# Performance work log

Measured on AMD Instinct MI355X. Metric: run time of the kernel, lower is better.

The kernel has to match this reference:

```python
import jax, jax.numpy as jnp
import numpy as np

B, N, T, DIN = 64, 512, 8, 2
H, L, E, M, P = 256, 3, 8192, 128, 12
EPS = 1e-5


def setup_inputs() -> dict:
    key = jax.random.key(0)
    ks = jax.random.split(key, 10)
    obs_traj = jax.random.normal(ks[0], (B, N, T, DIN), dtype=jnp.float32)
    nodes = jax.random.randint(ks[1], (B, 1, E), 0, N)
    edges = jax.random.randint(ks[2], (B, 1, E), 0, M)
    hyperedge_indices = jnp.concatenate([nodes, edges], axis=1)  # [B,2,E]
    s = 0.05
    return {
        "obs_traj": obs_traj,
        "hyperedge_indices": hyperedge_indices,
        "W_enc": jax.random.normal(ks[3], (DIN, H), dtype=jnp.float32) * s,
        "b_enc": jnp.zeros((H,), dtype=jnp.float32),
        "thetas": jax.random.normal(ks[4], (L, H, H), dtype=jnp.float32) * s,
        "conv_biases": jnp.zeros((L, H), dtype=jnp.float32),
        "gammas": jnp.ones((L, H), dtype=jnp.float32),
        "betas": jnp.zeros((L, H), dtype=jnp.float32),
        "W_dec": jax.random.normal(ks[5], (H, P * 2), dtype=jnp.float32) * s,
        "b_dec": jnp.zeros((P * 2,), dtype=jnp.float32),
    }


def _hconv(x, idx, theta, bias):
    # PyG HypergraphConv: out = D^{-1} H B^{-1} H^T (X Theta) + bias
    # x: [N,H], idx: [2,E] (row0 node ids, row1 hyperedge ids)
    nodes, edges = idx[0], idx[1]
    xt = x @ theta  # [N,H]
    ones = jnp.ones((idx.shape[1],), dtype=x.dtype)
    b_deg = jax.ops.segment_sum(ones, edges, num_segments=M)  # hyperedge degree [M]
    d_deg = jax.ops.segment_sum(ones, nodes, num_segments=N)  # node degree [N]
    msg = jax.ops.segment_sum(xt[nodes], edges, num_segments=M)  # [M,H]
    msg = msg / jnp.maximum(b_deg, 1.0)[:, None]
    out = jax.ops.segment_sum(msg[edges], nodes, num_segments=N)  # [N,H]
    out = out / jnp.maximum(d_deg, 1.0)[:, None]
    return out + bias


def reference(obs_traj, hyperedge_indices, W_enc, b_enc, thetas, conv_biases,
              gammas, betas, W_dec, b_dec):
    # TemporalEncoder: per-step linear + ReLU, mean over time -> [B,N,H]
    h = jnp.mean(jax.nn.relu(obs_traj @ W_enc + b_enc), axis=2)
    h_social = h
    for l in range(L):
        conv = jax.vmap(lambda x, idx: _hconv(x, idx, thetas[l], conv_biases[l]))
        hc = conv(h_social, hyperedge_indices)  # [B,N,H]
        # BatchNorm1d applied per sample (training-mode stats over node dim)
        mu = jnp.mean(hc, axis=1, keepdims=True)
        var = jnp.var(hc, axis=1, keepdims=True)
        hn = (hc - mu) * jax.lax.rsqrt(var + EPS) * gammas[l] + betas[l]
        h_social = jax.nn.relu(hn)  # dropout = identity (eval)
    h_combined = h + h_social
    out = h_combined @ W_dec + b_dec  # [B,N,P*2]
    return out.reshape(B, N, P, 2)
```

## Files before the change

kernel.cpp:

```cpp
#include <hip/hip_runtime.h>
#include <hip/hip_bf16.h>

#define B_   64
#define N_   512
#define T_   8
#define DIN_ 2
#define H_   256
#define L_   3
#define E_   8192
#define M_   128
#define P2_  24
#define EPS_ 1e-5f

#define WTPAD 136

typedef __attribute__((ext_vector_type(8))) short short8;
typedef __attribute__((ext_vector_type(4))) float floatx4;

__device__ __forceinline__ unsigned short f2bf(float f) {
    union { float f; unsigned u; } v; v.f = f;
    unsigned r = v.u + 0x7FFF + ((v.u >> 16) & 1);
    return (unsigned short)(r >> 16);
}
__device__ __forceinline__ float bf2f(unsigned short h) {
    union { unsigned u; float f; } v; v.u = (unsigned)h << 16; return v.f;
}

__global__ __launch_bounds__(512, 4) void prep_kernel(
    const float* __restrict__ obs, const float* __restrict__ Wenc,
    const float* __restrict__ benc,
    unsigned short* __restrict__ actT, long actLo,
    const int* __restrict__ idx, unsigned short* __restrict__ Hmat,
    unsigned short* __restrict__ HmatT, float* __restrict__ DinvN,
    float* __restrict__ degM,
    const float* __restrict__ thetas, unsigned short* __restrict__ thT, long thLo)
{
    __shared__ __align__(16) char u[33024];
    int bid = blockIdx.x, tid = threadIdx.x;
    if (bid < 256) {
        float* ot = (float*)u;
        int x8 = bid & 7, s = bid >> 3;
        int b = ((s >> 2) << 3) | x8;
        int h0 = (s & 3) * 64;
        const float4* src = (const float4*)(obs + (long)b * N_ * 16);
        for (int i = tid; i < 2048; i += 512) {
            float4 v = src[i];
            int n = i >> 2, k4 = (i & 3) << 2;
            ot[(k4 + 0) * 513 + n] = v.x;
            ot[(k4 + 1) * 513 + n] = v.y;
            ot[(k4 + 2) * 513 + n] = v.z;
            ot[(k4 + 3) * 513 + n] = v.w;
        }
        __syncthreads();
        int wave = tid >> 6, lane = tid & 63;
        int cbase = h0 + wave * 8;
        float w0[8], w1[8], bb[8];
#pragma unroll
        for (int i = 0; i < 8; ++i) {
            w0[i] = Wenc[cbase + i];
            w1[i] = Wenc[H_ + cbase + i];
            bb[i] = benc[cbase + i];
        }
        for (int j = 0; j < 8; ++j) {
            int n = j * 64 + lane;
            float x0[8], x1[8];
#pragma unroll
            for (int t = 0; t < 8; ++t) {
                x0[t] = ot[(2 * t) * 513 + n];
                x1[t] = ot[(2 * t + 1) * 513 + n];
            }
#pragma unroll
            for (int i = 0; i < 8; ++i) {
                float acc = 0.f;
#pragma unroll
                for (int t = 0; t < 8; ++t)
                    acc += fmaxf(x0[t] * w0[i] + x1[t] * w1[i] + bb[i], 0.f);
                acc *= 0.125f;
                long o = ((long)b * H_ + cbase + i) * N_ + n;
                unsigned short hv = f2bf(acc);
                actT[o] = hv;
                actT[actLo + o] = f2bf(acc - bf2f(hv));
            }
        }
    } else if (bid < 768) {
        unsigned* cnt = (unsigned*)u;
        int id2 = bid - 256;
        int x8 = id2 & 7, s = id2 >> 3;
        int b = ((s >> 3) << 3) | x8;
        int chunk = s & 7;
        int c0 = chunk * 64;
        for (int i = tid; i < 64 * 129; i += 512) cnt[i] = 0;
        __syncthreads();
        const int* nodes = idx + (long)b * 2 * E_;
        const int* edges = nodes + E_;
        for (int e = tid; e < E_; e += 512) {
            int n = nodes[e];
            if ((n >> 6) == chunk) atomicAdd(&cnt[(n & 63) * 129 + edges[e]], 1u);
        }
        __syncthreads();
        for (int i = tid; i < 64 * 128; i += 512) {
            int r = i >> 7, m = i & 127;
            Hmat[((long)(b * N_ + c0 + r)) * M_ + m] = f2bf((float)cnt[r * 129 + m]);
        }
        for (int i = tid; i < 64 * 128; i += 512) {
            int m = i >> 6, r = i & 63;
            HmatT[((long)(b * M_ + m)) * N_ + c0 + r] = f2bf((float)cnt[r * 129 + m]);
        }
        if (tid < 64) {
            unsigned s2 = 0;
#pragma unroll 8
            for (int m = 0; m < 128; ++m) s2 += cnt[tid * 129 + m];
            DinvN[b * N_ + c0 + tid] = 1.0f / fmaxf((float)s2, 1.0f);
        } else if (tid < 192) {
            int m = tid - 64;
            unsigned s2 = 0;
#pragma unroll 8
            for (int r = 0; r < 64; ++r) s2 += cnt[r * 129 + m];
            atomicAdd(&degM[b * M_ + m], (float)s2);
        }
    } else {
        float (*tile)[65] = (float(*)[65])u;
        int sub = bid - 768;
        int cx = sub & 3, ry = (sub >> 2) & 3, l = sub >> 4;
        int r0 = ry * 64, c0 = cx * 64;
        const float* ib = thetas + (long)l * H_ * H_;
        unsigned short* ob = thT + (long)l * H_ * H_;
        int x = tid & 63, y0 = tid >> 6;
#pragma unroll
        for (int i = 0; i < 8; ++i) {
            int y = y0 * 8 + i;
            tile[y][x] = ib[(long)(r0 + y) * H_ + c0 + x];
        }
        __syncthreads();
#pragma unroll
        for (int i = 0; i < 8; ++i) {
            int y = y0 * 8 + i;
            float v = tile[x][y];
            unsigned short hv = f2bf(v);
            long o = (long)(c0 + y) * H_ + r0 + x;
            ob[o] = hv;
            ob[thLo + o] = f2bf(v - bf2f(hv));
        }
    }
}

__global__ __launch_bounds__(256, 4) void z_kernel(
    const unsigned short* __restrict__ HmatT,
    const unsigned short* __restrict__ actIn, long actLo,
    const float* __restrict__ degM,
    unsigned short* __restrict__ Zg, long zLo)
{
    __shared__ __align__(16) unsigned short As1[128 * 40];
    __shared__ __align__(16) unsigned short Bh[64 * 40];
    __shared__ __align__(16) unsigned short Bl[64 * 40];
    int b = blockIdx.x, hs = blockIdx.y * 64;
    int tid = threadIdx.x, wave = tid >> 6, lane = tid & 63;
    int lr = lane & 15, lq = lane >> 4;
    int wm = (wave & 1) * 64, wn = (wave >> 1) * 32;
    const unsigned short* HT   = HmatT + (long)b * M_ * N_;
    const unsigned short* aInH = actIn + (long)b * H_ * N_ + (long)hs * N_;
    const unsigned short* aInL = actIn + actLo + (long)b * H_ * N_ + (long)hs * N_;

    floatx4 acc[4][2] = {};
    int r0 = tid >> 2, ck = (tid & 3) << 3;
    int r1 = r0 + 64;
    uint4 pA0 = *(const uint4*)&HT[(long)r0 * N_ + ck];
    uint4 pA1 = *(const uint4*)&HT[(long)r1 * N_ + ck];
    uint4 pBh = *(const uint4*)&aInH[(long)r0 * N_ + ck];
    uint4 pBl = *(const uint4*)&aInL[(long)r0 * N_ + ck];
    for (int k0 = 0; k0 < N_; k0 += 32) {
        __syncthreads();
        *(uint4*)&As1[r0 * 40 + ck] = pA0;
        *(uint4*)&As1[r1 * 40 + ck] = pA1;
        *(uint4*)&Bh[r0 * 40 + ck]  = pBh;
        *(uint4*)&Bl[r0 * 40 + ck]  = pBl;
        __syncthreads();
        int kn = k0 + 32;
        if (kn < N_) {
            pA0 = *(const uint4*)&HT[(long)r0 * N_ + kn + ck];
            pA1 = *(const uint4*)&HT[(long)r1 * N_ + kn + ck];
            pBh = *(const uint4*)&aInH[(long)r0 * N_ + kn + ck];
            pBl = *(const uint4*)&aInL[(long)r0 * N_ + kn + ck];
        }
        short8 af[4], bh[2], bl[2];
#pragma unroll
        for (int mt = 0; mt < 4; ++mt)
            af[mt] = *(const short8*)&As1[(wm + mt * 16 + lr) * 40 + lq * 8];
#pragma unroll
        for (int nt = 0; nt < 2; ++nt) {
            bh[nt] = *(const short8*)&Bh[(wn + nt * 16 + lr) * 40 + lq * 8];
            bl[nt] = *(const short8*)&Bl[(wn + nt * 16 + lr) * 40 + lq * 8];
        }
#pragma unroll
        for (int mt = 0; mt < 4; ++mt)
#pragma unroll
            for (int nt = 0; nt < 2; ++nt) {
                acc[mt][nt] = __builtin_amdgcn_mfma_f32_16x16x32_bf16(
                    af[mt], bh[nt], acc[mt][nt], 0, 0, 0);
                acc[mt][nt] = __builtin_amdgcn_mfma_f32_16x16x32_bf16(
                    af[mt], bl[nt], acc[mt][nt], 0, 0, 0);
            }
    }
#pragma unroll
    for (int mt = 0; mt < 4; ++mt)
#pragma unroll
        for (int r4 = 0; r4 < 4; ++r4) {
            int m = wm + mt * 16 + lq * 4 + r4;
            float rsB = 1.0f / fmaxf(degM[b * M_ + m], 1.0f);
#pragma unroll
            for (int nt = 0; nt < 2; ++nt) {
                float v = acc[mt][nt][r4] * rsB;
                unsigned short hv = f2bf(v);
                long o = ((long)b * M_ + m) * H_ + hs + wn + nt * 16 + lr;
                Zg[o] = hv;
                Zg[zLo + o] = f2bf(v - bf2f(hv));
            }
        }
}

__global__ __launch_bounds__(512, 4) void wh_kernel(
    const unsigned short* __restrict__ Zg, long zLo,
    const unsigned short* __restrict__ Hmat,
    const unsigned short* __restrict__ thT, long thLo,
    const float* __restrict__ DinvN, const float* __restrict__ convb,
    const float* __restrict__ gamma, const float* __restrict__ beta,
    unsigned short* __restrict__ actOut, long actLo)
{
    __shared__ __align__(16) char lds[28160];
    unsigned short* Zch  = (unsigned short*)lds;
    unsigned short* Zcl  = Zch + 128 * 40;
    unsigned short* As2h = Zcl + 128 * 40;
    unsigned short* As2l = As2h + 32 * 40;
    unsigned short* Wh   = (unsigned short*)lds;
    unsigned short* Wl   = Wh + 32 * WTPAD;
    float* rsum = (float*)(lds + 25600);
    float* rsq  = rsum + 256;
    float2* prm = (float2*)(rsq + 256);

    int id = blockIdx.x;
    int xcd = id & 7, slot = id >> 3;
    int chunk = slot & 7;
    int b  = ((slot >> 3) << 3) | xcd;
    int h0 = chunk * 32;

    int tid = threadIdx.x, wave = tid >> 6, lane = tid & 63;
    int lr = lane & 15, lq = lane >> 4;
    const unsigned short* Zb = Zg + (long)b * M_ * H_;
    const unsigned short* Hm = Hmat + (long)b * N_ * M_;

    int wm2 = (wave >> 2) * 16, wn2 = (wave & 3) * 32;
    int i2 = tid & 255, pl2 = tid >> 8;
    int r2 = i2 >> 2, ck2 = (i2 & 3) << 3;
    bool thAct = (i2 < 128);
    const unsigned short* thBase = thT + (pl2 ? thLo : 0) + (long)(h0 + r2) * H_ + ck2;
    unsigned short* As2dst = (pl2 ? As2l : As2h) + r2 * 40 + ck2;
    int rz = tid >> 2, ckz = (tid & 3) << 3;
    uint4 pTh = {};
    if (thAct) pTh = *(const uint4*)thBase;
    uint4 pZh = *(const uint4*)&Zb[(long)rz * H_ + ckz];
    uint4 pZl = *(const uint4*)&Zb[zLo + (long)rz * H_ + ckz];
    floatx4 acc2[2] = {};
    for (int k0 = 0; k0 < H_; k0 += 32) {
        __syncthreads();
        if (thAct) *(uint4*)As2dst = pTh;
        *(uint4*)&Zch[rz * 40 + ckz] = pZh;
        *(uint4*)&Zcl[rz * 40 + ckz] = pZl;
        __syncthreads();
        int kn = k0 + 32;
        if (kn < H_) {
            if (thAct) pTh = *(const uint4*)(thBase + kn);
            pZh = *(const uint4*)&Zb[(long)rz * H_ + kn + ckz];
            pZl = *(const uint4*)&Zb[zLo + (long)rz * H_ + kn + ckz];
        }
        short8 ah, al, zb[2], zl[2];
        ah = *(const short8*)&As2h[(wm2 + lr) * 40 + lq * 8];
        al = *(const short8*)&As2l[(wm2 + lr) * 40 + lq * 8];
#pragma unroll
        for (int nt = 0; nt < 2; ++nt) {
            zb[nt] = *(const short8*)&Zch[(wn2 + nt * 16 + lr) * 40 + lq * 8];
            zl[nt] = *(const short8*)&Zcl[(wn2 + nt * 16 + lr) * 40 + lq * 8];
        }
#pragma unroll
        for (int nt = 0; nt < 2; ++nt) {
            acc2[nt] = __builtin_amdgcn_mfma_f32_16x16x32_bf16(ah, zb[nt], acc2[nt], 0, 0, 0);
            acc2[nt] = __builtin_amdgcn_mfma_f32_16x16x32_bf16(ah, zl[nt], acc2[nt], 0, 0, 0);
            acc2[nt] = __builtin_amdgcn_mfma_f32_16x16x32_bf16(al, zb[nt], acc2[nt], 0, 0, 0);
        }
    }
    __syncthreads();
#pragma unroll
    for (int r4 = 0; r4 < 4; ++r4) {
        int row = wm2 + lq * 4 + r4;
#pragma unroll
        for (int nt = 0; nt < 2; ++nt) {
            int col = wn2 + nt * 16 + lr;
            float v = acc2[nt][r4];
            unsigned short hv = f2bf(v);
            Wh[row * WTPAD + col] = hv;
            Wl[row * WTPAD + col] = f2bf(v - bf2f(hv));
        }
    }
    __syncthreads();

    int wn3 = wave * 64;
    floatx4 acc3[2][4] = {};
    for (int k0 = 0; k0 < M_; k0 += 32) {
        short8 ah[2], al[2], bh3[4];
#pragma unroll
        for (int nt = 0; nt < 4; ++nt)
            bh3[nt] = *(const short8*)&Hm[(long)(wn3 + nt * 16 + lr) * M_ + k0 + lq * 8];
#pragma unroll
        for (int mt = 0; mt < 2; ++mt) {
            ah[mt] = *(const short8*)&Wh[(mt * 16 + lr) * WTPAD + k0 + lq * 8];
            al[mt] = *(const short8*)&Wl[(mt * 16 + lr) * WTPAD + k0 + lq * 8];
        }
#pragma unroll
        for (int mt = 0; mt < 2; ++mt)
#pragma unroll
            for (int nt = 0; nt < 4; ++nt) {
                acc3[mt][nt] = __builtin_amdgcn_mfma_f32_16x16x32_bf16(
                    ah[mt], bh3[nt], acc3[mt][nt], 0, 0, 0);
                acc3[mt][nt] = __builtin_amdgcn_mfma_f32_16x16x32_bf16(
                    al[mt], bh3[nt], acc3[mt][nt], 0, 0, 0);
            }
    }

    float dv[4];
#pragma unroll
    for (int nt = 0; nt < 4; ++nt)
        dv[nt] = DinvN[b * N_ + wn3 + nt * 16 + lr];
    float cb[2][4];
#pragma unroll
    for (int mt = 0; mt < 2; ++mt)
#pragma unroll
        for (int r4 = 0; r4 < 4; ++r4)
            cb[mt][r4] = convb[h0 + mt * 16 + lq * 4 + r4];
#pragma unroll
    for (int mt = 0; mt < 2; ++mt)
#pragma unroll
        for (int nt = 0; nt < 4; ++nt)
#pragma unroll
            for (int r4 = 0; r4 < 4; ++r4)
                acc3[mt][nt][r4] = acc3[mt][nt][r4] * dv[nt] + cb[mt][r4];

    float ps[2][4], pq[2][4];
#pragma unroll
    for (int mt = 0; mt < 2; ++mt)
#pragma unroll
        for (int r4 = 0; r4 < 4; ++r4) {
            float s = 0.f, q = 0.f;
#pragma unroll
            for (int nt = 0; nt < 4; ++nt) {
                float v = acc3[mt][nt][r4];
                s += v; q += v * v;
            }
            ps[mt][r4] = s; pq[mt][r4] = q;
        }
#pragma unroll
    for (int mask = 1; mask <= 8; mask <<= 1) {
#pragma unroll
        for (int mt = 0; mt < 2; ++mt)
#pragma unroll
            for (int r4 = 0; r4 < 4; ++r4) {
                ps[mt][r4] += __shfl_xor(ps[mt][r4], mask);
                pq[mt][r4] += __shfl_xor(pq[mt][r4], mask);
            }
    }
    if (lr == 0) {
#pragma unroll
        for (int mt = 0; mt < 2; ++mt)
#pragma unroll
            for (int r4 = 0; r4 < 4; ++r4) {
                int row = mt * 16 + lq * 4 + r4;
                rsum[row * 8 + wave] = ps[mt][r4];
                rsq[row * 8 + wave]  = pq[mt][r4];
            }
    }
    __syncthreads();
    if (tid < 32) {
        float s = 0.f, s2 = 0.f;
#pragma unroll
        for (int w = 0; w < 8; ++w) { s += rsum[tid * 8 + w]; s2 += rsq[tid * 8 + w]; }
        float mu  = s * (1.0f / N_);
        float var = fmaxf(s2 * (1.0f / N_) - mu * mu, 0.f);
        float sc  = gamma[h0 + tid] * rsqrtf(var + EPS_);
        prm[tid] = make_float2(sc, beta[h0 + tid] - mu * sc);
    }
    __syncthreads();

    unsigned short* ab = actOut + (long)b * H_ * N_;
#pragma unroll
    for (int mt = 0; mt < 2; ++mt)
#pragma unroll
        for (int r4 = 0; r4 < 4; ++r4) {
            int row = mt * 16 + lq * 4 + r4;
            float2 p = prm[row];
#pragma unroll
            for (int nt = 0; nt < 4; ++nt) {
                float y = fmaxf(acc3[mt][nt][r4] * p.x + p.y, 0.f);
                unsigned short hv = f2bf(y);
                long o = (long)(h0 + row) * N_ + wn3 + nt * 16 + lr;
                ab[o] = hv;
                ab[actLo + o] = f2bf(y - bf2f(hv));
            }
        }
}

__global__ __launch_bounds__(256, 2) void decoder_kernel(
    const unsigned short* __restrict__ hAct,
    const unsigned short* __restrict__ sAct,
    const float* __restrict__ Wdec, const float* __restrict__ bdec,
    float* __restrict__ out)
{
    __shared__ float ct[64 * 65];
    __shared__ float wd[256 * 25];
    int n0 = blockIdx.x * 64, b = blockIdx.y;
    int tid = threadIdx.x;
    for (int i = tid; i < 256 * 24; i += 256)
        wd[(i / 24) * 25 + (i % 24)] = Wdec[i];

    const unsigned short* hb = hAct + (long)b * H_ * N_;
    const unsigned short* sb = sAct + (long)b * H_ * N_;
    int x = tid & 63, y0 = tid >> 6;

    int n = tid >> 2;
    int p0 = (tid & 3) * 6;
    float acc[6] = {};

    for (int k0 = 0; k0 < H_; k0 += 64) {
        __syncthreads();
#pragma unroll
        for (int i = 0; i < 16; ++i) {
            int y = y0 * 16 + i;
            long o = (long)(k0 + y) * N_ + n0 + x;
            ct[x * 65 + y] = bf2f(hb[o]) + bf2f(sb[o]);
        }
        __syncthreads();
        const float* crow = &ct[n * 65];
#pragma unroll 8
        for (int kk = 0; kk < 64; ++kk) {
            float a = crow[kk];
            const float* wrow = &wd[(k0 + kk) * 25 + p0];
#pragma unroll
            for (int j = 0; j < 6; ++j)
                acc[j] += a * wrow[j];
        }
    }
    long ob = ((long)b * N_ + n0 + n) * P2_ + p0;
#pragma unroll
    for (int j = 0; j < 6; ++j)
        out[ob + j] = acc[j] + bdec[p0 + j];
}

extern "C" void kernel_launch(void* const* d_in, const int* in_sizes, int n_in,
                              void* d_out, int out_size, void* d_ws, size_t ws_size,
                              hipStream_t stream) {
    const float* obs    = (const float*)d_in[0];
    const int*   hyper  = (const int*)d_in[1];
    const float* Wenc   = (const float*)d_in[2];
    const float* benc   = (const float*)d_in[3];
    const float* thetas = (const float*)d_in[4];
    const float* convb  = (const float*)d_in[5];
    const float* gammas = (const float*)d_in[6];
    const float* betas  = (const float*)d_in[7];
    const float* Wdec   = (const float*)d_in[8];
    const float* bdec   = (const float*)d_in[9];
    float* out = (float*)d_out;

    char* w = (char*)d_ws;
    auto alloc = [&](size_t bytes) { char* p = w; w += (bytes + 255) & ~255ULL; return p; };
    float* DinvN = (float*)alloc((size_t)B_ * N_ * 4);
    float* degM  = (float*)alloc((size_t)B_ * M_ * 4);
    unsigned short* Hmat  = (unsigned short*)alloc((size_t)B_ * N_ * M_ * 2);
    unsigned short* HmatT = (unsigned short*)alloc((size_t)B_ * M_ * N_ * 2);
    unsigned short* act0  = (unsigned short*)alloc((size_t)B_ * H_ * N_ * 2 * 2);
    unsigned short* act1  = (unsigned short*)alloc((size_t)B_ * H_ * N_ * 2 * 2);
    unsigned short* act2  = (unsigned short*)alloc((size_t)B_ * H_ * N_ * 2 * 2);
    unsigned short* thT   = (unsigned short*)alloc((size_t)L_ * H_ * H_ * 2 * 2);
    unsigned short* Zg    = (unsigned short*)alloc((size_t)B_ * M_ * H_ * 2 * 2);

    const long actLo = (long)B_ * H_ * N_;
    const long thLo  = (long)L_ * H_ * H_;
    const long zLo   = (long)B_ * M_ * H_;

    hipMemsetAsync(degM, 0, (size_t)B_ * M_ * 4, stream);
    prep_kernel<<<816, 512, 0, stream>>>(
        obs, Wenc, benc, act0, actLo,
        hyper, Hmat, HmatT, DinvN, degM,
        thetas, thT, thLo);

    unsigned short* bufs[4] = { act0, act1, act2, act1 };
    for (int l = 0; l < L_; ++l) {
        z_kernel<<<dim3(B_, 4), 256, 0, stream>>>(
            HmatT, bufs[l], actLo, degM, Zg, zLo);
        wh_kernel<<<512, 512, 0, stream>>>(
            Zg, zLo, Hmat, thT + (size_t)l * H_ * H_, thLo,
            DinvN, convb + (size_t)l * H_,
            gammas + (size_t)l * H_, betas + (size_t)l * H_, bufs[l + 1], actLo);
    }
    decoder_kernel<<<dim3(8, B_), 256, 0, stream>>>(
        act0, bufs[L_], Wdec, bdec, out);
}
```

Baseline: 225.5 us.

## Fuse all stages into one persistent kernel with software grid barriers

```diff
diff --git a/kernel.cpp b/kernel.cpp
--- a/kernel.cpp
+++ b/kernel.cpp
@@ -13,6 +13,7 @@
 #define EPS_ 1e-5f
 
 #define WTPAD 136
+#define NBLK 512
 
 typedef __attribute__((ext_vector_type(8))) short short8;
 typedef __attribute__((ext_vector_type(4))) float floatx4;
@@ -26,430 +27,435 @@
     union { unsigned u; float f; } v; v.u = (unsigned)h << 16; return v.f;
 }
 
-__global__ __launch_bounds__(512, 4) void prep_kernel(
+__global__ __launch_bounds__(512, 4) void mega_kernel(
     const float* __restrict__ obs, const float* __restrict__ Wenc,
-    const float* __restrict__ benc,
-    unsigned short* __restrict__ actT, long actLo,
-    const int* __restrict__ idx, unsigned short* __restrict__ Hmat,
-    unsigned short* __restrict__ HmatT, float* __restrict__ DinvN,
-    float* __restrict__ degM,
-    const float* __restrict__ thetas, unsigned short* __restrict__ thT, long thLo)
+    const float* __restrict__ benc, const int* __restrict__ idx,
+    const float* __restrict__ thetas, const float* __restrict__ convb,
+    const float* __restrict__ gammas, const float* __restrict__ betas,
+    const float* __restrict__ Wdec, const float* __restrict__ bdec,
+    unsigned short* __restrict__ Hmat, unsigned short* __restrict__ HmatT,
+    float* __restrict__ DinvN, float* __restrict__ degM,
+    unsigned short* __restrict__ act0, unsigned short* __restrict__ act1,
+    unsigned short* __restrict__ act2, long actLo,
+    unsigned short* __restrict__ thT, long thLo,
+    unsigned short* __restrict__ Zg, long zLo,
+    unsigned* __restrict__ cnt, float* __restrict__ out)
 {
-    __shared__ __align__(16) char u[33024];
+    __shared__ __align__(16) char u[43008];
     int bid = blockIdx.x, tid = threadIdx.x;
-    if (bid < 256) {
-        float* ot = (float*)u;
-        int x8 = bid & 7, s = bid >> 3;
-        int b = ((s >> 2) << 3) | x8;
-        int h0 = (s & 3) * 64;
-        const float4* src = (const float4*)(obs + (long)b * N_ * 16);
-        for (int i = tid; i < 2048; i += 512) {
-            float4 v = src[i];
-            int n = i >> 2, k4 = (i & 3) << 2;
-            ot[(k4 + 0) * 513 + n] = v.x;
-            ot[(k4 + 1) * 513 + n] = v.y;
-            ot[(k4 + 2) * 513 + n] = v.z;
-            ot[(k4 + 3) * 513 + n] = v.w;
+    int wave = tid >> 6, lane = tid & 63;
+    int lr = lane & 15, lq = lane >> 4;
+    unsigned target = 0;
+
+    auto gbar = [&]() {
+        __syncthreads();
+        target += NBLK;
+        if (tid == 0) {
+            __threadfence();
+            atomicAdd(cnt, 1u);
+            while (atomicAdd(cnt, 0u) < target) __builtin_amdgcn_s_sleep(2);
+            __threadfence();
         }
         __syncthreads();
-        int wave = tid >> 6, lane = tid & 63;
-        int cbase = h0 + wave * 8;
-        float w0[8], w1[8], bb[8];
-#pragma unroll
-        for (int i = 0; i < 8; ++i) {
-            w0[i] = Wenc[cbase + i];
-            w1[i] = Wenc[H_ + cbase + i];
-            bb[i] = benc[cbase + i];
-        }
-        for (int j = 0; j < 8; ++j) {
-            int n = j * 64 + lane;
-            float x0[8], x1[8];
-#pragma unroll
-            for (int t = 0; t < 8; ++t) {
-                x0[t] = ot[(2 * t) * 513 + n];
-                x1[t] = ot[(2 * t + 1) * 513 + n];
-            }
+    };
+
+    for (int pass = 0; pass < 2; ++pass) {
+        int role = (pass == 0) ? bid : (bid < 304 ? 512 + bid : -1);
+        if (role < 0) break;
+        __syncthreads();
+        if (role < 256) {
+            float* ot = (float*)u;
+            int x8 = role & 7, s = role >> 3;
+            int b = ((s >> 2) << 3) | x8;
+            int h0 = (s & 3) * 64;
+            const float4* src = (const float4*)(obs + (long)b * N_ * 16);
+            for (int i = tid; i < 2048; i += 512) {
+                float4 v = src[i];
+                int n = i >> 2, k4 = (i & 3) << 2;
+                ot[(k4 + 0) * 513 + n] = v.x;
+                ot[(k4 + 1) * 513 + n] = v.y;
+                ot[(k4 + 2) * 513 + n] = v.z;
+                ot[(k4 + 3) * 513 + n] = v.w;
+            }
+            __syncthreads();
+            int cbase = h0 + wave * 8;
+            float w0[8], w1[8], bb[8];
 #pragma unroll
             for (int i = 0; i < 8; ++i) {
-                float acc = 0.f;
-#pragma unroll
-                for (int t = 0; t < 8; ++t)
-                    acc += fmaxf(x0[t] * w0[i] + x1[t] * w1[i] + bb[i], 0.f);
-                acc *= 0.125f;
-                long o = ((long)b * H_ + cbase + i) * N_ + n;
-                unsigned short hv = f2bf(acc);
-                actT[o] = hv;
-                actT[actLo + o] = f2bf(acc - bf2f(hv));
-            }
-        }
-    } else if (bid < 768) {
-        unsigned* cnt = (unsigned*)u;
-        int id2 = bid - 256;
-        int x8 = id2 & 7, s = id2 >> 3;
-        int b = ((s >> 3) << 3) | x8;
-        int chunk = s & 7;
-        int c0 = chunk * 64;
-        for (int i = tid; i < 64 * 129; i += 512) cnt[i] = 0;
-        __syncthreads();
-        const int* nodes = idx + (long)b * 2 * E_;
-        const int* edges = nodes + E_;
-        for (int e = tid; e < E_; e += 512) {
-            int n = nodes[e];
-            if ((n >> 6) == chunk) atomicAdd(&cnt[(n & 63) * 129 + edges[e]], 1u);
-        }
-        __syncthreads();
-        for (int i = tid; i < 64 * 128; i += 512) {
-            int r = i >> 7, m = i & 127;
-            Hmat[((long)(b * N_ + c0 + r)) * M_ + m] = f2bf((float)cnt[r * 129 + m]);
-        }
-        for (int i = tid; i < 64 * 128; i += 512) {
-            int m = i >> 6, r = i & 63;
-            HmatT[((long)(b * M_ + m)) * N_ + c0 + r] = f2bf((float)cnt[r * 129 + m]);
-        }
-        if (tid < 64) {
-            unsigned s2 = 0;
+                w0[i] = Wenc[cbase + i];
+                w1[i] = Wenc[H_ + cbase + i];
+                bb[i] = benc[cbase + i];
+            }
+            for (int j = 0; j < 8; ++j) {
+                int n = j * 64 + lane;
+                float x0[8], x1[8];
+#pragma unroll
+                for (int t = 0; t < 8; ++t) {
+                    x0[t] = ot[(2 * t) * 513 + n];
+                    x1[t] = ot[(2 * t + 1) * 513 + n];
+                }
+#pragma unroll
+                for (int i = 0; i < 8; ++i) {
+                    float acc = 0.f;
+#pragma unroll
+                    for (int t = 0; t < 8; ++t)
+                        acc += fmaxf(x0[t] * w0[i] + x1[t] * w1[i] + bb[i], 0.f);
+                    acc *= 0.125f;
+                    long o = ((long)b * H_ + cbase + i) * N_ + n;
+                    unsigned short hv = f2bf(acc);
+                    act0[o] = hv;
+                    act0[actLo + o] = f2bf(acc - bf2f(hv));
+                }
+            }
+        } else if (role < 768) {
+            unsigned* cw = (unsigned*)u;
+            int id2 = role - 256;
+            int x8 = id2 & 7, s = id2 >> 3;
+            int b = ((s >> 3) << 3) | x8;
+            int chunk = s & 7;
+            int c0 = chunk * 64;
+            for (int i = tid; i < 64 * 129; i += 512) cw[i] = 0;
+            __syncthreads();
+            const int* nodes = idx + (long)b * 2 * E_;
+            const int* edges = nodes + E_;
+            for (int e = tid; e < E_; e += 512) {
+                int n = nodes[e];
+                if ((n >> 6) == chunk) atomicAdd(&cw[(n & 63) * 129 + edges[e]], 1u);
+            }
+            __syncthreads();
+            for (int i = tid; i < 64 * 128; i += 512) {
+                int r = i >> 7, m = i & 127;
+                Hmat[((long)(b * N_ + c0 + r)) * M_ + m] = f2bf((float)cw[r * 129 + m]);
+            }
+            for (int i = tid; i < 64 * 128; i += 512) {
+                int m = i >> 6, r = i & 63;
+                HmatT[((long)(b * M_ + m)) * N_ + c0 + r] = f2bf((float)cw[r * 129 + m]);
+            }
+            if (tid < 64) {
+                unsigned s2 = 0;
 #pragma unroll 8
-            for (int m = 0; m < 128; ++m) s2 += cnt[tid * 129 + m];
-            DinvN[b * N_ + c0 + tid] = 1.0f / fmaxf((float)s2, 1.0f);
-        } else if (tid < 192) {
-            int m = tid - 64;
-            unsigned s2 = 0;
+                for (int m = 0; m < 128; ++m) s2 += cw[tid * 129 + m];
+                DinvN[b * N_ + c0 + tid] = 1.0f / fmaxf((float)s2, 1.0f);
+            } else if (tid < 192) {
+                int m = tid - 64;
+                unsigned s2 = 0;
 #pragma unroll 8
-            for (int r = 0; r < 64; ++r) s2 += cnt[r * 129 + m];
-            atomicAdd(&degM[b * M_ + m], (float)s2);
-        }
-    } else {
-        float (*tile)[65] = (float(*)[65])u;
-        int sub = bid - 768;
-        int cx = sub & 3, ry = (sub >> 2) & 3, l = sub >> 4;
-        int r0 = ry * 64, c0 = cx * 64;
-        const float* ib = thetas + (long)l * H_ * H_;
-        unsigned short* ob = thT + (long)l * H_ * H_;
-        int x = tid & 63, y0 = tid >> 6;
-#pragma unroll
-        for (int i = 0; i < 8; ++i) {
-            int y = y0 * 8 + i;
-            tile[y][x] = ib[(long)(r0 + y) * H_ + c0 + x];
-        }
-        __syncthreads();
-#pragma unroll
-        for (int i = 0; i < 8; ++i) {
-            int y = y0 * 8 + i;
-            float v = tile[x][y];
-            unsigned short hv = f2bf(v);
-            long o = (long)(c0 + y) * H_ + r0 + x;
-            ob[o] = hv;
-            ob[thLo + o] = f2bf(v - bf2f(hv));
+                for (int r = 0; r < 64; ++r) s2 += cw[r * 129 + m];
+                atomicAdd(&degM[b * M_ + m], (float)s2);
+            }
+        } else {
+            float (*tile)[65] = (float(*)[65])u;
+            int sub = role - 768;
+            int cx = sub & 3, ry = (sub >> 2) & 3, l = sub >> 4;
+            int r0 = ry * 64, c0 = cx * 64;
+            const float* ib = thetas + (long)l * H_ * H_;
+            unsigned short* ob = thT + (long)l * H_ * H_;
+            int x = tid & 63, y0 = tid >> 6;
+#pragma unroll
+            for (int i = 0; i < 8; ++i) {
+                int y = y0 * 8 + i;
+                tile[y][x] = ib[(long)(r0 + y) * H_ + c0 + x];
+            }
+            __syncthreads();
+#pragma unroll
+            for (int i = 0; i < 8; ++i) {
+                int y = y0 * 8 + i;
+                float v = tile[x][y];
+                unsigned short hv = f2bf(v);
+                long o = (long)(c0 + y) * H_ + r0 + x;
+                ob[o] = hv;
+                ob[thLo + o] = f2bf(v - bf2f(hv));
+            }
         }
     }
-}
-
-__global__ __launch_bounds__(256, 4) void z_kernel(
-    const unsigned short* __restrict__ HmatT,
-    const unsigned short* __restrict__ actIn, long actLo,
-    const float* __restrict__ degM,
-    unsigned short* __restrict__ Zg, long zLo)
-{
-    __shared__ __align__(16) unsigned short As1[128 * 40];
-    __shared__ __align__(16) unsigned short Bh[64 * 40];
-    __shared__ __align__(16) unsigned short Bl[64 * 40];
-    int b = blockIdx.x, hs = blockIdx.y * 64;
-    int tid = threadIdx.x, wave = tid >> 6, lane = tid & 63;
-    int lr = lane & 15, lq = lane >> 4;
-    int wm = (wave & 1) * 64, wn = (wave >> 1) * 32;
-    const unsigned short* HT   = HmatT + (long)b * M_ * N_;
-    const unsigned short* aInH = actIn + (long)b * H_ * N_ + (long)hs * N_;
-    const unsigned short* aInL = actIn + actLo + (long)b * H_ * N_ + (long)hs * N_;
-
-    floatx4 acc[4][2] = {};
-    int r0 = tid >> 2, ck = (tid & 3) << 3;
-    int r1 = r0 + 64;
-    uint4 pA0 = *(const uint4*)&HT[(long)r0 * N_ + ck];
-    uint4 pA1 = *(const uint4*)&HT[(long)r1 * N_ + ck];
-    uint4 pBh = *(const uint4*)&aInH[(long)r0 * N_ + ck];
-    uint4 pBl = *(const uint4*)&aInL[(long)r0 * N_ + ck];
-    for (int k0 = 0; k0 < N_; k0 += 32) {
-        __syncthreads();
-        *(uint4*)&As1[r0 * 40 + ck] = pA0;
-        *(uint4*)&As1[r1 * 40 + ck] = pA1;
-        *(uint4*)&Bh[r0 * 40 + ck]  = pBh;
-        *(uint4*)&Bl[r0 * 40 + ck]  = pBl;
-        __syncthreads();
-        int kn = k0 + 32;
-        if (kn < N_) {
-            pA0 = *(const uint4*)&HT[(long)r0 * N_ + kn + ck];
-            pA1 = *(const uint4*)&HT[(long)r1 * N_ + kn + ck];
-            pBh = *(const uint4*)&aInH[(long)r0 * N_ + kn + ck];
-            pBl = *(const uint4*)&aInL[(long)r0 * N_ + kn + ck];
+    gbar();
+
+    unsigned short* bufs[4] = { act0, act1, act2, act1 };
+    for (int l = 0; l < L_; ++l) {
+        {
+            unsigned short* As1 = (unsigned short*)u;
+            unsigned short* Bh  = As1 + 128 * 40;
+            unsigned short* Bl  = Bh + 32 * 40;
+            int x8 = bid & 7, slot = bid >> 3;
+            int b = ((slot >> 3) << 3) | x8;
+            int hs = (slot & 7) * 32;
+            const unsigned short* HT = HmatT + (long)b * M_ * N_;
+            const unsigned short* aH = bufs[l] + (long)b * H_ * N_ + (long)hs * N_;
+            const unsigned short* aL = bufs[l] + actLo + (long)b * H_ * N_ + (long)hs * N_;
+            int wm = (wave & 3) * 32, wn16 = (wave >> 2) * 16;
+            floatx4 acc[2] = {};
+            bool isA = tid < 256;
+            int r0 = (tid & 255) >> 2, c0 = (tid & 3) << 3;
+            int jb = tid - 256, plb = (jb >> 7) & 1, jj = jb & 127;
+            int rb = jj >> 2, cbb = (jj & 3) << 3;
+            uint4 pa0 = {}, pa1 = {}, pb = {};
+            if (isA) {
+                pa0 = *(const uint4*)&HT[(long)r0 * N_ + c0];
+                pa1 = *(const uint4*)&HT[(long)(r0 + 64) * N_ + c0];
+            } else {
+                pb = *(const uint4*)&(plb ? aL : aH)[(long)rb * N_ + cbb];
+            }
+            for (int k0 = 0; k0 < N_; k0 += 32) {
+                __syncthreads();
+                if (isA) {
+                    *(uint4*)&As1[r0 * 40 + c0] = pa0;
+                    *(uint4*)&As1[(r0 + 64) * 40 + c0] = pa1;
+                } else {
+                    *(uint4*)&(plb ? Bl : Bh)[rb * 40 + cbb] = pb;
+                }
+                __syncthreads();
+                int kn = k0 + 32;
+                if (kn < N_) {
+                    if (isA) {
+                        pa0 = *(const uint4*)&HT[(long)r0 * N_ + kn + c0];
+                        pa1 = *(const uint4*)&HT[(long)(r0 + 64) * N_ + kn + c0];
+                    } else {
+                        pb = *(const uint4*)&(plb ? aL : aH)[(long)rb * N_ + kn + cbb];
+                    }
+                }
+                short8 af0 = *(const short8*)&As1[(wm + lr) * 40 + lq * 8];
+                short8 af1 = *(const short8*)&As1[(wm + 16 + lr) * 40 + lq * 8];
+                short8 fb  = *(const short8*)&Bh[(wn16 + lr) * 40 + lq * 8];
+                short8 fl  = *(const short8*)&Bl[(wn16 + lr) * 40 + lq * 8];
+                acc[0] = __builtin_amdgcn_mfma_f32_16x16x32_bf16(af0, fb, acc[0], 0, 0, 0);
+                acc[0] = __builtin_amdgcn_mfma_f32_16x16x32_bf16(af0, fl, acc[0], 0, 0, 0);
+                acc[1] = __builtin_amdgcn_mfma_f32_16x16x32_bf16(af1, fb, acc[1], 0, 0, 0);
+                acc[1] = __builtin_amdgcn_mfma_f32_16x16x32_bf16(af1, fl, acc[1], 0, 0, 0);
+            }
+#pragma unroll
+            for (int mt = 0; mt < 2; ++mt)
+#pragma unroll
+                for (int r4 = 0; r4 < 4; ++r4) {
+                    int m = wm + mt * 16 + lq * 4 + r4;
+                    float rsB = 1.0f / fmaxf(degM[b * M_ + m], 1.0f);
+                    float v = acc[mt][r4] * rsB;
+                    unsigned short hv = f2bf(v);
+                    long o = ((long)b * M_ + m) * H_ + hs + wn16 + lr;
+                    Zg[o] = hv;
+                    Zg[zLo + o] = f2bf(v - bf2f(hv));
+                }
         }
-        short8 af[4], bh[2], bl[2];
-#pragma unroll
-        for (int mt = 0; mt < 4; ++mt)
-            af[mt] = *(const short8*)&As1[(wm + mt * 16 + lr) * 40 + lq * 8];
-#pragma unroll
-        for (int nt = 0; nt < 2; ++nt) {
-            bh[nt] = *(const short8*)&Bh[(wn + nt * 16 + lr) * 40 + lq * 8];
-            bl[nt] = *(const short8*)&Bl[(wn + nt * 16 + lr) * 40 + lq * 8];
+        gbar();
+
+        {
+            unsigned short* Zch  = (unsigned short*)u;
+            unsigned short* Zcl  = Zch + 128 * 40;
+            unsigned short* As2h = Zcl + 128 * 40;
+            unsigned short* As2l = As2h + 32 * 40;
+            unsigned short* Wh   = (unsigned short*)u;
+            unsigned short* Wl   = Wh + 32 * WTPAD;
+            float* rsum = (float*)(u + 25600);
+            float* rsq  = rsum + 256;
+            float2* prm = (float2*)(rsq + 256);
+
+            int xcd = bid & 7, slot = bid >> 3;
+            int chunk = slot & 7;
+            int b  = ((slot >> 3) << 3) | xcd;
+            int h0 = chunk * 32;
+            const unsigned short* Zb = Zg + (long)b * M_ * H_;
+            const unsigned short* Hm = Hmat + (long)b * N_ * M_;
+            const unsigned short* thTl = thT + (size_t)l * H_ * H_;
+            const float* cbv = convb + (size_t)l * H_;
+            const float* gmv = gammas + (size_t)l * H_;
+            const float* btv = betas + (size_t)l * H_;
+            unsigned short* actOut = bufs[l + 1];
+
+            int wm2 = (wave >> 2) * 16, wn2 = (wave & 3) * 32;
+            int i2 = tid & 255, pl2 = tid >> 8;
+            int r2 = i2 >> 2, ck2 = (i2 & 3) << 3;
+            bool thAct = (i2 < 128);
+            const unsigned short* thBase = thTl + (pl2 ? thLo : 0) + (long)(h0 + r2) * H_ + ck2;
+            unsigned short* As2dst = (pl2 ? As2l : As2h) + r2 * 40 + ck2;
+            int rz = tid >> 2, ckz = (tid & 3) << 3;
+            uint4 pTh = {};
+            if (thAct) pTh = *(const uint4*)thBase;
+            uint4 pZh = *(const uint4*)&Zb[(long)rz * H_ + ckz];
+            uint4 pZl = *(const uint4*)&Zb[zLo + (long)rz * H_ + ckz];
+            floatx4 acc2[2] = {};
+            for (int k0 = 0; k0 < H_; k0 += 32) {
+                __syncthreads();
+                if (thAct) *(uint4*)As2dst = pTh;
+                *(uint4*)&Zch[rz * 40 + ckz] = pZh;
+                *(uint4*)&Zcl[rz * 40 + ckz] = pZl;
+                __syncthreads();
+                int kn = k0 + 32;
+                if (kn < H_) {
+                    if (thAct) pTh = *(const uint4*)(thBase + kn);
+                    pZh = *(const uint4*)&Zb[(long)rz * H_ + kn + ckz];
+                    pZl = *(const uint4*)&Zb[zLo + (long)rz * H_ + kn + ckz];
+                }
+                short8 ah, al, zb[2], zl[2];
+                ah = *(const short8*)&As2h[(wm2 + lr) * 40 + lq * 8];
+                al = *(const short8*)&As2l[(wm2 + lr) * 40 + lq * 8];
+#pragma unroll
+                for (int nt = 0; nt < 2; ++nt) {
+                    zb[nt] = *(const short8*)&Zch[(wn2 + nt * 16 + lr) * 40 + lq * 8];
+                    zl[nt] = *(const short8*)&Zcl[(wn2 + nt * 16 + lr) * 40 + lq * 8];
+                }
+#pragma unroll
+                for (int nt = 0; nt < 2; ++nt) {
+                    acc2[nt] = __builtin_amdgcn_mfma_f32_16x16x32_bf16(ah, zb[nt], acc2[nt], 0, 0, 0);
+                    acc2[nt] = __builtin_amdgcn_mfma_f32_16x16x32_bf16(ah, zl[nt], acc2[nt], 0, 0, 0);
+                    acc2[nt] = __builtin_amdgcn_mfma_f32_16x16x32_bf16(al, zb[nt], acc2[nt], 0, 0, 0);
+                }
+            }
+            __syncthreads();
+#pragma unroll
+            for (int r4 = 0; r4 < 4; ++r4) {
+                int row = wm2 + lq * 4 + r4;
+#pragma unroll
+                for (int nt = 0; nt < 2; ++nt) {
+                    int col = wn2 + nt * 16 + lr;
+                    float v = acc2[nt][r4];
+                    unsigned short hv = f2bf(v);
+                    Wh[row * WTPAD + col] = hv;
+                    Wl[row * WTPAD + col] = f2bf(v - bf2f(hv));
+                }
+            }
+            __syncthreads();
+
+            int wn3 = wave * 64;
+            floatx4 acc3[2][4] = {};
+            for (int k0 = 0; k0 < M_; k0 += 32) {
+                short8 ah[2], al[2], bh3[4];
+#pragma unroll
+                for (int nt = 0; nt < 4; ++nt)
+                    bh3[nt] = *(const short8*)&Hm[(long)(wn3 + nt * 16 + lr) * M_ + k0 + lq * 8];
+#pragma unroll
+                for (int mt = 0; mt < 2; ++mt) {
+                    ah[mt] = *(const short8*)&Wh[(mt * 16 + lr) * WTPAD + k0 + lq * 8];
+                    al[mt] = *(const short8*)&Wl[(mt * 16 + lr) * WTPAD + k0 + lq * 8];
+                }
+#pragma unroll
+                for (int mt = 0; mt < 2; ++mt)
+#pragma unroll
+                    for (int nt = 0; nt < 4; ++nt) {
+                        acc3[mt][nt] = __builtin_amdgcn_mfma_f32_16x16x32_bf16(
+                            ah[mt], bh3[nt], acc3[mt][nt], 0, 0, 0);
+                        acc3[mt][nt] = __builtin_amdgcn_mfma_f32_16x16x32_bf16(
+                            al[mt], bh3[nt], acc3[mt][nt], 0, 0, 0);
+                    }
+            }
+
+            float dv[4];
+#pragma unroll
+            for (int nt = 0; nt < 4; ++nt)
+                dv[nt] = DinvN[b * N_ + wn3 + nt * 16 + lr];
+            float cb2[2][4];
+#pragma unroll
+            for (int mt = 0; mt < 2; ++mt)
+#pragma unroll
+                for (int r4 = 0; r4 < 4; ++r4)
+                    cb2[mt][r4] = cbv[h0 + mt * 16 + lq * 4 + r4];
+#pragma unroll
+            for (int mt = 0; mt < 2; ++mt)
+#pragma unroll
+                for (int nt = 0; nt < 4; ++nt)
+#pragma unroll
+                    for (int r4 = 0; r4 < 4; ++r4)
+                        acc3[mt][nt][r4] = acc3[mt][nt][r4] * dv[nt] + cb2[mt][r4];
+
+            float ps[2][4], pq[2][4];
+#pragma unroll
+            for (int mt = 0; mt < 2; ++mt)
+#pragma unroll
+                for (int r4 = 0; r4 < 4; ++r4) {
+                    float s = 0.f, q = 0.f;
+#pragma unroll
+                    for (int nt = 0; nt < 4; ++nt) {
+                        float v = acc3[mt][nt][r4];
+                        s += v; q += v * v;
+                    }
+                    ps[mt][r4] = s; pq[mt][r4] = q;
+                }
+#pragma unroll
+            for (int mask = 1; mask <= 8; mask <<= 1) {
+#pragma unroll
+                for (int mt = 0; mt < 2; ++mt)
+#pragma unroll
+                    for (int r4 = 0; r4 < 4; ++r4) {
+                        ps[mt][r4] += __shfl_xor(ps[mt][r4], mask);
+                        pq[mt][r4] += __shfl_xor(pq[mt][r4], mask);
+                    }
+            }
+            if (lr == 0) {
+#pragma unroll
+                for (int mt = 0; mt < 2; ++mt)
+#pragma unroll
+                    for (int r4 = 0; r4 < 4; ++r4) {
+                        int row = mt * 16 + lq * 4 + r4;
+                        rsum[row * 8 + wave] = ps[mt][r4];
+                        rsq[row * 8 + wave]  = pq[mt][r4];
+                    }
+            }
+            __syncthreads();
+            if (tid < 32) {
+                float s = 0.f, s2 = 0.f;
+#pragma unroll
+                for (int w2 = 0; w2 < 8; ++w2) { s += rsum[tid * 8 + w2]; s2 += rsq[tid * 8 + w2]; }
+                float mu  = s * (1.0f / N_);
+                float var = fmaxf(s2 * (1.0f / N_) - mu * mu, 0.f);
+                float sc  = gmv[h0 + tid] * rsqrtf(var + EPS_);
+                prm[tid] = make_float2(sc, btv[h0 + tid] - mu * sc);
+            }
+            __syncthreads();
+
+            unsigned short* ab = actOut + (long)b * H_ * N_;
+#pragma unroll
+            for (int mt = 0; mt < 2; ++mt)
+#pragma unroll
+                for (int r4 = 0; r4 < 4; ++r4) {
+                    int row = mt * 16 + lq * 4 + r4;
+                    float2 p = prm[row];
+#pragma unroll
+                    for (int nt = 0; nt < 4; ++nt) {
+                        float y = fmaxf(acc3[mt][nt][r4] * p.x + p.y, 0.f);
+                        unsigned short hv = f2bf(y);
+                        long o = (long)(h0 + row) * N_ + wn3 + nt * 16 + lr;
+                        ab[o] = hv;
+                        ab[actLo + o] = f2bf(y - bf2f(hv));
+                    }
+                }
         }
-#pragma unroll
-        for (int mt = 0; mt < 4; ++mt)
-#pragma unroll
-            for (int nt = 0; nt < 2; ++nt) {
-                acc[mt][nt] = __builtin_amdgcn_mfma_f32_16x16x32_bf16(
-                    af[mt], bh[nt], acc[mt][nt], 0, 0, 0);
-                acc[mt][nt] = __builtin_amdgcn_mfma_f32_16x16x32_bf16(
-                    af[mt], bl[nt], acc[mt][nt], 0, 0, 0);
-            }
+        gbar();
     }
-#pragma unroll
-    for (int mt = 0; mt < 4; ++mt)
-#pragma unroll
-        for (int r4 = 0; r4 < 4; ++r4) {
-            int m = wm + mt * 16 + lq * 4 + r4;
-            float rsB = 1.0f / fmaxf(degM[b * M_ + m], 1.0f);
-#pragma unroll
-            for (int nt = 0; nt < 2; ++nt) {
-                float v = acc[mt][nt][r4] * rsB;
-                unsigned short hv = f2bf(v);
-                long o = ((long)b * M_ + m) * H_ + hs + wn + nt * 16 + lr;
-                Zg[o] = hv;
-                Zg[zLo + o] = f2bf(v - bf2f(hv));
+
+    {
+        float* ct = (float*)u;
+        float* wd = ct + 64 * 65;
+        int n0 = (bid & 7) * 64, b = bid >> 3;
+        for (int i = tid; i < 256 * 24; i += 512)
+            wd[(i / 24) * 25 + (i % 24)] = Wdec[i];
+        const unsigned short* hb = act0 + (long)b * H_ * N_;
+        const unsigned short* sb = bufs[L_] + (long)b * H_ * N_;
+        int x = tid & 63, y0 = tid >> 6;
+        int n = tid >> 3;
+        int p0 = (tid & 7) * 3;
+        float acc[3] = {};
+        for (int k0 = 0; k0 < H_; k0 += 64) {
+            __syncthreads();
+#pragma unroll
+            for (int i = 0; i < 8; ++i) {
+                int y = y0 * 8 + i;
+                long o = (long)(k0 + y) * N_ + n0 + x;
+                ct[x * 65 + y] = bf2f(hb[o]) + bf2f(sb[o]);
+            }
+            __syncthreads();
+            const float* crow = &ct[n * 65];
+#pragma unroll 8
+            for (int kk = 0; kk < 64; ++kk) {
+                float a = crow[kk];
+                const float* wrow = &wd[(k0 + kk) * 25 + p0];
+                acc[0] += a * wrow[0];
+                acc[1] += a * wrow[1];
+                acc[2] += a * wrow[2];
             }
         }
-}
-
-__global__ __launch_bounds__(512, 4) void wh_kernel(
-    const unsigned short* __restrict__ Zg, long zLo,
-    const unsigned short* __restrict__ Hmat,
-    const unsigned short* __restrict__ thT, long thLo,
-    const float* __restrict__ DinvN, const float* __restrict__ convb,
-    const float* __restrict__ gamma, const float* __restrict__ beta,
-    unsigned short* __restrict__ actOut, long actLo)
-{
-    __shared__ __align__(16) char lds[28160];
-    unsigned short* Zch  = (unsigned short*)lds;
-    unsigned short* Zcl  = Zch + 128 * 40;
-    unsigned short* As2h = Zcl + 128 * 40;
-    unsigned short* As2l = As2h + 32 * 40;
-    unsigned short* Wh   = (unsigned short*)lds;
-    unsigned short* Wl   = Wh + 32 * WTPAD;
-    float* rsum = (float*)(lds + 25600);
-    float* rsq  = rsum + 256;
-    float2* prm = (float2*)(rsq + 256);
-
-    int id = blockIdx.x;
-    int xcd = id & 7, slot = id >> 3;
-    int chunk = slot & 7;
-    int b  = ((slot >> 3) << 3) | xcd;
-    int h0 = chunk * 32;
-
-    int tid = threadIdx.x, wave = tid >> 6, lane = tid & 63;
-    int lr = lane & 15, lq = lane >> 4;
-    const unsigned short* Zb = Zg + (long)b * M_ * H_;
-    const unsigned short* Hm = Hmat + (long)b * N_ * M_;
-
-    int wm2 = (wave >> 2) * 16, wn2 = (wave & 3) * 32;
-    int i2 = tid & 255, pl2 = tid >> 8;
-    int r2 = i2 >> 2, ck2 = (i2 & 3) << 3;
-    bool thAct = (i2 < 128);
-    const unsigned short* thBase = thT + (pl2 ? thLo : 0) + (long)(h0 + r2) * H_ + ck2;
-    unsigned short* As2dst = (pl2 ? As2l : As2h) + r2 * 40 + ck2;
-    int rz = tid >> 2, ckz = (tid & 3) << 3;
-    uint4 pTh = {};
-    if (thAct) pTh = *(const uint4*)thBase;
-    uint4 pZh = *(const uint4*)&Zb[(long)rz * H_ + ckz];
-    uint4 pZl = *(const uint4*)&Zb[zLo + (long)rz * H_ + ckz];
-    floatx4 acc2[2] = {};
-    for (int k0 = 0; k0 < H_; k0 += 32) {
-        __syncthreads();
-        if (thAct) *(uint4*)As2dst = pTh;
-        *(uint4*)&Zch[rz * 40 + ckz] = pZh;
-        *(uint4*)&Zcl[rz * 40 + ckz] = pZl;
-        __syncthreads();
-        int kn = k0 + 32;
-        if (kn < H_) {
-            if (thAct) pTh = *(const uint4*)(thBase + kn);
-            pZh = *(const uint4*)&Zb[(long)rz * H_ + kn + ckz];
-            pZl = *(const uint4*)&Zb[zLo + (long)rz * H_ + kn + ckz];
-        }
-        short8 ah, al, zb[2], zl[2];
-        ah = *(const short8*)&As2h[(wm2 + lr) * 40 + lq * 8];
-        al = *(const short8*)&As2l[(wm2 + lr) * 40 + lq * 8];
-#pragma unroll
-        for (int nt = 0; nt < 2; ++nt) {
-            zb[nt] = *(const short8*)&Zch[(wn2 + nt * 16 + lr) * 40 + lq * 8];
-            zl[nt] = *(const short8*)&Zcl[(wn2 + nt * 16 + lr) * 40 + lq * 8];
-        }
-#pragma unroll
-        for (int nt = 0; nt < 2; ++nt) {
-            acc2[nt] = __builtin_amdgcn_mfma_f32_16x16x32_bf16(ah, zb[nt], acc2[nt], 0, 0, 0);
-            acc2[nt] = __builtin_amdgcn_mfma_f32_16x16x32_bf16(ah, zl[nt], acc2[nt], 0, 0, 0);
-            acc2[nt] = __builtin_amdgcn_mfma_f32_16x16x32_bf16(al, zb[nt], acc2[nt], 0, 0, 0);
-        }
+        long ob = ((long)b * N_ + n0 + n) * P2_ + p0;
+        out[ob + 0] = acc[0] + bdec[p0 + 0];
+        out[ob + 1] = acc[1] + bdec[p0 + 1];
+        out[ob + 2] = acc[2] + bdec[p0 + 2];
     }
-    __syncthreads();
-#pragma unroll
-    for (int r4 = 0; r4 < 4; ++r4) {
-        int row = wm2 + lq * 4 + r4;
-#pragma unroll
-        for (int nt = 0; nt < 2; ++nt) {
-            int col = wn2 + nt * 16 + lr;
-            float v = acc2[nt][r4];
-            unsigned short hv = f2bf(v);
-            Wh[row * WTPAD + col] = hv;
-            Wl[row * WTPAD + col] = f2bf(v - bf2f(hv));
-        }
-    }
-    __syncthreads();
-
-    int wn3 = wave * 64;
-    floatx4 acc3[2][4] = {};
-    for (int k0 = 0; k0 < M_; k0 += 32) {
-        short8 ah[2], al[2], bh3[4];
-#pragma unroll
-        for (int nt = 0; nt < 4; ++nt)
-            bh3[nt] = *(const short8*)&Hm[(long)(wn3 + nt * 16 + lr) * M_ + k0 + lq * 8];
-#pragma unroll
-        for (int mt = 0; mt < 2; ++mt) {
-            ah[mt] = *(const short8*)&Wh[(mt * 16 + lr) * WTPAD + k0 + lq * 8];
-            al[mt] = *(const short8*)&Wl[(mt * 16 + lr) * WTPAD + k0 + lq * 8];
-        }
-#pragma unroll
-        for (int mt = 0; mt < 2; ++mt)
-#pragma unroll
-            for (int nt = 0; nt < 4; ++nt) {
-                acc3[mt][nt] = __builtin_amdgcn_mfma_f32_16x16x32_bf16(
-                    ah[mt], bh3[nt], acc3[mt][nt], 0, 0, 0);
-                acc3[mt][nt] = __builtin_amdgcn_mfma_f32_16x16x32_bf16(
-                    al[mt], bh3[nt], acc3[mt][nt], 0, 0, 0);
-            }
-    }
-
-    float dv[4];
-#pragma unroll
-    for (int nt = 0; nt < 4; ++nt)
-        dv[nt] = DinvN[b * N_ + wn3 + nt * 16 + lr];
-    float cb[2][4];
-#pragma unroll
-    for (int mt = 0; mt < 2; ++mt)
-#pragma unroll
-        for (int r4 = 0; r4 < 4; ++r4)
-            cb[mt][r4] = convb[h0 + mt * 16 + lq * 4 + r4];
-#pragma unroll
-    for (int mt = 0; mt < 2; ++mt)
-#pragma unroll
-        for (int nt = 0; nt < 4; ++nt)
-#pragma unroll
-            for (int r4 = 0; r4 < 4; ++r4)
-                acc3[mt][nt][r4] = acc3[mt][nt][r4] * dv[nt] + cb[mt][r4];
-
-    float ps[2][4], pq[2][4];
-#pragma unroll
-    for (int mt = 0; mt < 2; ++mt)
-#pragma unroll
-        for (int r4 = 0; r4 < 4; ++r4) {
-            float s = 0.f, q = 0.f;
-#pragma unroll
-            for (int nt = 0; nt < 4; ++nt) {
-                float v = acc3[mt][nt][r4];
-                s += v; q += v * v;
-            }
-            ps[mt][r4] = s; pq[mt][r4] = q;
-        }
-#pragma unroll
-    for (int mask = 1; mask <= 8; mask <<= 1) {
-#pragma unroll
-        for (int mt = 0; mt < 2; ++mt)
-#pragma unroll
-            for (int r4 = 0; r4 < 4; ++r4) {
-                ps[mt][r4] += __shfl_xor(ps[mt][r4], mask);
-                pq[mt][r4] += __shfl_xor(pq[mt][r4], mask);
-            }
-    }
-    if (lr == 0) {
-#pragma unroll
-        for (int mt = 0; mt < 2; ++mt)
-#pragma unroll
-            for (int r4 = 0; r4 < 4; ++r4) {
-                int row = mt * 16 + lq * 4 + r4;
-                rsum[row * 8 + wave] = ps[mt][r4];
-                rsq[row * 8 + wave]  = pq[mt][r4];
-            }
-    }
-    __syncthreads();
-    if (tid < 32) {
-        float s = 0.f, s2 = 0.f;
-#pragma unroll
-        for (int w = 0; w < 8; ++w) { s += rsum[tid * 8 + w]; s2 += rsq[tid * 8 + w]; }
-        float mu  = s * (1.0f / N_);
-        float var = fmaxf(s2 * (1.0f / N_) - mu * mu, 0.f);
-        float sc  = gamma[h0 + tid] * rsqrtf(var + EPS_);
-        prm[tid] = make_float2(sc, beta[h0 + tid] - mu * sc);
-    }
-    __syncthreads();
-
-    unsigned short* ab = actOut + (long)b * H_ * N_;
-#pragma unroll
-    for (int mt = 0; mt < 2; ++mt)
-#pragma unroll
-        for (int r4 = 0; r4 < 4; ++r4) {
-            int row = mt * 16 + lq * 4 + r4;
-            float2 p = prm[row];
-#pragma unroll
-            for (int nt = 0; nt < 4; ++nt) {
-                float y = fmaxf(acc3[mt][nt][r4] * p.x + p.y, 0.f);
-                unsigned short hv = f2bf(y);
-                long o = (long)(h0 + row) * N_ + wn3 + nt * 16 + lr;
-                ab[o] = hv;
-                ab[actLo + o] = f2bf(y - bf2f(hv));
-            }
-        }
-}
-
-__global__ __launch_bounds__(256, 2) void decoder_kernel(
-    const unsigned short* __restrict__ hAct,
-    const unsigned short* __restrict__ sAct,
-    const float* __restrict__ Wdec, const float* __restrict__ bdec,
-    float* __restrict__ out)
-{
-    __shared__ float ct[64 * 65];
-    __shared__ float wd[256 * 25];
-    int n0 = blockIdx.x * 64, b = blockIdx.y;
-    int tid = threadIdx.x;
-    for (int i = tid; i < 256 * 24; i += 256)
-        wd[(i / 24) * 25 + (i % 24)] = Wdec[i];
-
-    const unsigned short* hb = hAct + (long)b * H_ * N_;
-    const unsigned short* sb = sAct + (long)b * H_ * N_;
-    int x = tid & 63, y0 = tid >> 6;
-
-    int n = tid >> 2;
-    int p0 = (tid & 3) * 6;
-    float acc[6] = {};
-
-    for (int k0 = 0; k0 < H_; k0 += 64) {
-        __syncthreads();
-#pragma unroll
-        for (int i = 0; i < 16; ++i) {
-            int y = y0 * 16 + i;
-            long o = (long)(k0 + y) * N_ + n0 + x;
-            ct[x * 65 + y] = bf2f(hb[o]) + bf2f(sb[o]);
-        }
-        __syncthreads();
-        const float* crow = &ct[n * 65];
-#pragma unroll 8
-        for (int kk = 0; kk < 64; ++kk) {
-            float a = crow[kk];
-            const float* wrow = &wd[(k0 + kk) * 25 + p0];
-#pragma unroll
-            for (int j = 0; j < 6; ++j)
-                acc[j] += a * wrow[j];
-        }
-    }
-    long ob = ((long)b * N_ + n0 + n) * P2_ + p0;
-#pragma unroll
-    for (int j = 0; j < 6; ++j)
-        out[ob + j] = acc[j] + bdec[p0 + j];
 }
 
 extern "C" void kernel_launch(void* const* d_in, const int* in_sizes, int n_in,
@@ -469,8 +475,9 @@
 
     char* w = (char*)d_ws;
     auto alloc = [&](size_t bytes) { char* p = w; w += (bytes + 255) & ~255ULL; return p; };
+    unsigned* cnt = (unsigned*)alloc(256);
+    float* degM  = (float*)alloc((size_t)B_ * M_ * 4);
     float* DinvN = (float*)alloc((size_t)B_ * N_ * 4);
-    float* degM  = (float*)alloc((size_t)B_ * M_ * 4);
     unsigned short* Hmat  = (unsigned short*)alloc((size_t)B_ * N_ * M_ * 2);
     unsigned short* HmatT = (unsigned short*)alloc((size_t)B_ * M_ * N_ * 2);
     unsigned short* act0  = (unsigned short*)alloc((size_t)B_ * H_ * N_ * 2 * 2);
@@ -483,21 +490,9 @@
     const long thLo  = (long)L_ * H_ * H_;
     const long zLo   = (long)B_ * M_ * H_;
 
-    hipMemsetAsync(degM, 0, (size_t)B_ * M_ * 4, stream);
-    prep_kernel<<<816, 512, 0, stream>>>(
-        obs, Wenc, benc, act0, actLo,
-        hyper, Hmat, HmatT, DinvN, degM,
-        thetas, thT, thLo);
-
-    unsigned short* bufs[4] = { act0, act1, act2, act1 };
-    for (int l = 0; l < L_; ++l) {
-        z_kernel<<<dim3(B_, 4), 256, 0, stream>>>(
-            HmatT, bufs[l], actLo, degM, Zg, zLo);
-        wh_kernel<<<512, 512, 0, stream>>>(
-            Zg, zLo, Hmat, thT + (size_t)l * H_ * H_, thLo,
-            DinvN, convb + (size_t)l * H_,
-            gammas + (size_t)l * H_, betas + (size_t)l * H_, bufs[l + 1], actLo);
-    }
-    decoder_kernel<<<dim3(8, B_), 256, 0, stream>>>(
-        act0, bufs[L_], Wdec, bdec, out);
+    hipMemsetAsync(cnt, 0, 256 + (size_t)B_ * M_ * 4, stream);
+    mega_kernel<<<NBLK, 512, 0, stream>>>(
+        obs, Wenc, benc, hyper, thetas, convb, gammas, betas, Wdec, bdec,
+        Hmat, HmatT, DinvN, degM, act0, act1, act2, actLo,
+        thT, thLo, Zg, zLo, cnt, out);
 }
```

After: 716.4 us. 218% more time.
